# Optimization experiments

Hardware: AMD Instinct MI355X
Metric: run time of the kernel (lower is better)

## Reference

```python
import jax, jax.numpy as jnp
import numpy as np
import math

H = 512        # hidden_dim
DEPTH = 5
KS = 3         # kernel size
DELTA = 0.1
M = 104        # timestamp == seq_len
NC = 5
B = 512
BN_EPS = 1e-5


def setup_inputs() -> dict:
    key = jax.random.key(0)
    ks = jax.random.split(key, 16)
    inp = {}
    inp['x'] = jax.random.normal(ks[0], (B, 1, M), dtype=jnp.float32)
    # CausalCNN: depth conv layers (first is 1->H, rest H->H), each followed by BN
    inp['conv_w0'] = jax.random.normal(ks[1], (H, 1, KS), dtype=jnp.float32) * (1.0 / np.sqrt(KS))
    inp['conv_b0'] = jnp.zeros((H,), jnp.float32)
    inp['conv_w'] = jax.random.normal(ks[2], (DEPTH - 1, H, H, KS), dtype=jnp.float32) * (1.0 / np.sqrt(H * KS))
    inp['conv_b'] = jnp.zeros((DEPTH - 1, H), jnp.float32)
    inp['bn_gamma'] = jnp.ones((DEPTH, H), jnp.float32)
    inp['bn_beta'] = jnp.zeros((DEPTH, H), jnp.float32)
    # input_proj
    inp['proj_w'] = jax.random.normal(ks[3], (H, H), dtype=jnp.float32) * (1.0 / np.sqrt(H))
    inp['proj_b'] = jnp.zeros((H,), jnp.float32)
    # ZOH layers: A = -0.01*I + 0.001*randn, B = 0.01*randn [H,1], C = 0.01*randn [1,H]
    eye = jnp.eye(H, dtype=jnp.float32)
    inp['A_all'] = -0.01 * eye[None] + 0.001 * jax.random.normal(ks[4], (DEPTH, H, H), dtype=jnp.float32)
    inp['B_all'] = 0.01 * jax.random.normal(ks[5], (DEPTH, H, 1), dtype=jnp.float32)
    inp['C_all'] = 0.01 * jax.random.normal(ks[6], (DEPTH, 1, H), dtype=jnp.float32)
    # fc_temp: Linear(H,H) -> BN1d(H) -> GELU -> Dropout(eval) -> Linear(H,NC)
    inp['fc1_w'] = jax.random.normal(ks[7], (H, H), dtype=jnp.float32) * (1.0 / np.sqrt(H))
    inp['fc1_b'] = jnp.zeros((H,), jnp.float32)
    inp['fc_bn_gamma'] = jnp.ones((H,), jnp.float32)
    inp['fc_bn_beta'] = jnp.zeros((H,), jnp.float32)
    inp['fc2_w'] = jax.random.normal(ks[8], (NC, H), dtype=jnp.float32) * (1.0 / np.sqrt(H))
    inp['fc2_b'] = jnp.zeros((NC,), jnp.float32)
    return inp


def _causal_conv(x, w, b):
    # x: [B, Cin, T], w: [Cout, Cin, K] -> left-pad K-1 (equivalent to pad both + trim right)
    y = jax.lax.conv_general_dilated(x, w, window_strides=(1,), padding=[(KS - 1, 0)],
                                     dimension_numbers=('NCH', 'OIH', 'NCH'))
    return y + b[None, :, None]


def _bn_ct(x, g, b):
    # BatchNorm1d over [B, C, T], batch statistics (training-mode normalization)
    m = x.mean(axis=(0, 2), keepdims=True)
    v = x.var(axis=(0, 2), keepdims=True)
    return g[None, :, None] * (x - m) * jax.lax.rsqrt(v + BN_EPS) + b[None, :, None]


def _pos_encoding(T, d):
    pos = jnp.arange(T, dtype=jnp.float32)[:, None]
    div = jnp.exp(jnp.arange(0, d, 2, dtype=jnp.float32) * (-math.log(10000.0) / d))
    pe = jnp.zeros((T, d), jnp.float32)
    pe = pe.at[:, 0::2].set(jnp.sin(pos * div))
    pe = pe.at[:, 1::2].set(jnp.cos(pos * div))
    return pe


def _zoh_kbar(A, Bv, Cv):
    # A: [H,H], Bv: [H,1], Cv: [1,H] -> normalized K_bar [M]
    A_bar = jax.scipy.linalg.expm(DELTA * A)
    I = jnp.eye(H, dtype=A.dtype)
    A_inv = jnp.linalg.inv(A + 0.001 * I)
    B_bar = A_inv @ (A_bar - I) @ (DELTA * Bv)  # [H,1]
    # term_k = C @ A_bar^k @ B_bar; sequential vector recurrence replaces matrix powers
    def step(v, _):
        term = (Cv @ v)[0, 0]
        return A_bar @ v, term
    _, terms = jax.lax.scan(step, B_bar, None, length=M)  # [M]
    Kb = jnp.flip(terms, axis=0)
    return Kb / (jnp.linalg.norm(Kb) + 1e-6)


def reference(x, conv_w0, conv_b0, conv_w, conv_b, bn_gamma, bn_beta, proj_w, proj_b,
              A_all, B_all, C_all, fc1_w, fc1_b, fc_bn_gamma, fc_bn_beta, fc2_w, fc2_b):
    # CausalCNN
    h = jax.nn.relu(_bn_ct(_causal_conv(x, conv_w0, conv_b0), bn_gamma[0], bn_beta[0]))
    for i in range(DEPTH - 1):
        h = jax.nn.relu(_bn_ct(_causal_conv(h, conv_w[i], conv_b[i]), bn_gamma[i + 1], bn_beta[i + 1]))
    h = jnp.transpose(h, (0, 2, 1))  # [B, T, H]
    # positional encoding + input projection
    h = h + _pos_encoding(M, H)[None]
    h = jnp.einsum('bth,oh->bto', h, proj_w) + proj_b
    # stacked ZOH kernels: each layer multiplies x by its normalized K_bar along time
    Ks = jax.vmap(_zoh_kbar)(A_all, B_all, C_all)  # [DEPTH, M]
    h = h * jnp.prod(Ks, axis=0)[None, :, None]
    # mean pool over time, then fc_temp (BN with batch stats, dropout = identity/eval)
    h = h.mean(axis=1)  # [B, H]
    h = jnp.dot(h, fc1_w.T) + fc1_b
    m = h.mean(axis=0, keepdims=True)
    v = h.var(axis=0, keepdims=True)
    h = fc_bn_gamma * (h - m) * jax.lax.rsqrt(v + BN_EPS) + fc_bn_beta
    h = jax.nn.gelu(h, approximate=False)
    logits = jnp.dot(h, fc2_w.T) + fc2_b  # [B, NC]
    return logits
```

## Files before the change

kernel.cpp:

```cpp
#include <hip/hip_runtime.h>
#include <cstdio>
#include <cmath>
#include <cstdint>

constexpr int BM = 512 * 104;
constexpr float BN_EPS = 1e-5f;

constexpr size_t SZ_BF   = (size_t)BM * 512 * 2;
constexpr size_t SZ_MAT5 = (size_t)5 * 512 * 512 * 4;
constexpr size_t OFF_YB0 = 0;
constexpr size_t OFF_YB1 = OFF_YB0 + SZ_BF;
constexpr size_t OFF_WT2 = OFF_YB1 + SZ_BF;
constexpr size_t OFF_X   = OFF_WT2 + 6291456;
constexpr size_t OFF_T1  = OFF_X   + SZ_MAT5;
constexpr size_t OFF_T2  = OFF_T1  + SZ_MAT5;
constexpr size_t OFF_E   = OFF_T2  + SZ_MAT5;
constexpr size_t OFF_MW  = OFF_E   + SZ_MAT5;
constexpr size_t OFF_P2  = OFF_MW  + SZ_MAT5;
constexpr size_t OFF_P4  = OFF_P2  + SZ_MAT5;
constexpr size_t OFF_ROWT= OFF_P4  + SZ_MAT5;
constexpr size_t OFF_COLS= OFF_ROWT + 655360;
constexpr size_t OFF_COLS2=OFF_COLS + 655360;
constexpr size_t OFF_PIVI= OFF_COLS2 + 655360;
constexpr size_t OFF_PJT = OFF_PIVI + 81920;
constexpr size_t OFF_F1T = OFF_PJT + 1048576;
constexpr size_t OFF_G   = OFF_F1T + 1048576;
constexpr size_t OFF_POOL= OFF_G   + 1048576;
constexpr size_t OFF_Z   = OFF_POOL + 1048576;
constexpr size_t OFF_ST  = OFF_Z   + 1048576;
constexpr size_t OFF_U   = OFF_ST  + 49152;
constexpr size_t OFF_SV  = OFF_U   + 10240;
constexpr size_t OFF_V   = OFF_SV  + 10240;
constexpr size_t OFF_WV  = OFF_V   + 81920;
constexpr size_t OFF_S   = OFF_WV  + 133120;
constexpr size_t WS_NEED = OFF_S + 512;

__device__ __forceinline__ float bf2f(unsigned short u) {
    union { uint32_t i; float f; } x; x.i = (uint32_t)u << 16; return x.f;
}
__device__ __forceinline__ unsigned short f2bf(float f) {
    union { float f; uint32_t i; } x; x.f = f;
    uint32_t r = x.i + 0x7FFFu + ((x.i >> 16) & 1u);
    return (unsigned short)(r >> 16);
}

typedef __bf16 bf16x8 __attribute__((ext_vector_type(8)));
typedef float  f32x4  __attribute__((ext_vector_type(4)));

__device__ __forceinline__ void gld16(const void* g, void* l) {
    __builtin_amdgcn_global_load_lds((const __attribute__((address_space(1))) uint32_t*)g,
                                     (__attribute__((address_space(3))) uint32_t*)l, 16, 0, 0);
}

__device__ __forceinline__ uint32_t bnrelu_pk(uint32_t u, float sc0, float sc1, float sh0, float sh1) {
    union { uint32_t i; float f; } a, b;
    a.i = u << 16;
    b.i = u & 0xFFFF0000u;
    float x0 = fmaxf(fmaf(a.f, sc0, sh0), 0.0f);
    float x1 = fmaxf(fmaf(b.f, sc1, sh1), 0.0f);
    uint32_t r;
    asm volatile("v_cvt_pk_bf16_f32 %0, %1, %2" : "=v"(r) : "v"(x0), "v"(x1));
    return r;
}

__global__ void k_pre(const float* __restrict__ W, unsigned short* __restrict__ Wt2,
                      const float* __restrict__ Aall, float* __restrict__ X, float* __restrict__ MW,
                      float* __restrict__ COLSa, const float* __restrict__ Call, float* __restrict__ WV,
                      const float* __restrict__ pin0, float* __restrict__ pout0,
                      const float* __restrict__ pin1, float* __restrict__ pout1,
                      const float* __restrict__ xin, const float* __restrict__ w0,
                      const float* __restrict__ b0, unsigned short* __restrict__ y0,
                      double* __restrict__ s1g, double* __restrict__ s2g)
{
    __shared__ float tile[64 * 68];
    int bid = blockIdx.x;
    int tid = threadIdx.x;
    if (bid < 2048) {
        int co = bid & 511, l = bid >> 9;
        const float* src = W + (long)(l * 512 + co) * 512 * 3;
        unsigned short* dst = Wt2 + (long)l * 3 * 262144 + ((long)co << 9);
        int v = (co >> 1) & 3;
#pragma unroll
        for (int q = 0; q < 2; ++q) {
            int ci = tid * 2 + q;
            int chunk = (ci >> 3) & 3;
            int di = (ci & ~31) + (((chunk ^ v) & 3) << 3) + (ci & 7);
            float f0 = src[ci * 3 + 0], f1 = src[ci * 3 + 1], f2 = src[ci * 3 + 2];
            dst[di] = f2bf(f0);
            dst[262144 + di] = f2bf(f1);
            dst[524288 + di] = f2bf(f2);
        }
        return;
    }
    if (bid < 7168) {
        long i = (long)(bid - 2048) * 256 + tid;
        float a = Aall[i];
        X[i] = 0.1f * a;
        int z = (int)(i >> 18);
        int rc = (int)(i & 262143);
        int r = rc >> 9, c = rc & 511;
        float mw = a + ((r == c) ? 0.001f : 0.0f);
        MW[i] = mw;
        if (c < 64) COLSa[(long)z * 32768 + r * 64 + c] = mw;
        if (i < 2560) WV[(i >> 9) * 6656 + (i & 511)] = Call[i];
        return;
    }
    if (bid < 7296) {
        int id = bid - 7168;
        int bx = id & 7, by = (id >> 3) & 7, zi = id >> 6;
        const float* in = zi ? pin1 : pin0;
        float* outp = zi ? pout1 : pout0;
        for (int it = 0; it < 4; ++it) {
            int s = it * 256 + tid;
            int r = s >> 4, c4 = (s & 15) * 4;
            *(float4*)&tile[r * 68 + c4] = *(const float4*)&in[(long)(bx * 64 + r) * 512 + by * 64 + c4];
        }
        __syncthreads();
        for (int it = 0; it < 4; ++it) {
            int s = it * 256 + tid;
            int r = s >> 4, c4 = (s & 15) * 4;
            float4 v;
            v.x = tile[(c4 + 0) * 68 + r];
            v.y = tile[(c4 + 1) * 68 + r];
            v.z = tile[(c4 + 2) * 68 + r];
            v.w = tile[(c4 + 3) * 68 + r];
            *(float4*)&outp[(long)(by * 64 + r) * 512 + bx * 64 + c4] = v;
        }
        return;
    }
    {
        int id = bid - 7296;
        int b = id & 511;
        int c = (id >> 9) * 256 + tid;
        float w_0 = w0[c * 3 + 0], w_1 = w0[c * 3 + 1], w_2 = w0[c * 3 + 2], bb = b0[c];
        const float* xb = xin + b * 104;
        unsigned short* yb = y0 + (long)b * 104 * 512 + c;
        float xm2 = 0.0f, xm1 = 0.0f;
        float s1 = 0.0f, s2 = 0.0f;
        for (int t = 0; t < 104; ++t) {
            float x0 = xb[t];
            float v = w_0 * xm2 + w_1 * xm1 + w_2 * x0 + bb;
            yb[t * 512] = f2bf(v);
            s1 += v; s2 += v * v;
            xm2 = xm1; xm1 = x0;
        }
        atomicAdd(&s1g[c], (double)s1);
        atomicAdd(&s2g[c], (double)s2);
    }
}

__global__ __launch_bounds__(256) void k_mm(
    const float* __restrict__ A, long sA, int lda,
    const float* __restrict__ Bm, long sB, int ldb,
    float* __restrict__ C, long sC, int ldc,
    int K, int mode,
    const float* __restrict__ aux, long sAux,
    const float* __restrict__ aux2, float* __restrict__ Cp,
    double* __restrict__ st1, double* __restrict__ st2, int pc)
{
    __shared__ float sm[2 * 32 * 68];
    float* As = sm;
    float* Bs = sm + 32 * 68;
    int z = blockIdx.z;
    A  += (long)z * sA;
    Bm += (long)z * sB;
    C  += (long)z * sC;
    if (aux) aux += (long)z * sAux;
    int m0 = blockIdx.x * 64, n0 = blockIdx.y * 64;
    int tid = threadIdx.x;
    int tx = tid & 15, ty = tid >> 4;
    float acc[4][4] = {};
    for (int k0 = 0; k0 < K; k0 += 32) {
        __syncthreads();
#pragma unroll
        for (int it = 0; it < 2; ++it) {
            int s = it * 256 + tid;
            int mm = s >> 3, k4 = (s & 7) * 4;
            float4 v = *(const float4*)&A[(long)(m0 + mm) * lda + k0 + k4];
            As[(k4 + 0) * 68 + mm] = v.x;
            As[(k4 + 1) * 68 + mm] = v.y;
            As[(k4 + 2) * 68 + mm] = v.z;
            As[(k4 + 3) * 68 + mm] = v.w;
        }
#pragma unroll
        for (int it = 0; it < 2; ++it) {
            int s = it * 256 + tid;
            int kk = s >> 4, n4 = (s & 15) * 4;
            *(float4*)&Bs[kk * 68 + n4] = *(const float4*)&Bm[(long)(k0 + kk) * ldb + n0 + n4];
        }
        __syncthreads();
#pragma unroll 8
        for (int kk = 0; kk < 32; ++kk) {
            float4 a = *(const float4*)&As[kk * 68 + ty * 4];
            float4 b = *(const float4*)&Bs[kk * 68 + tx * 4];
            float av[4] = {a.x, a.y, a.z, a.w};
            float bv[4] = {b.x, b.y, b.z, b.w};
#pragma unroll
            for (int i = 0; i < 4; ++i)
#pragma unroll
                for (int j = 0; j < 4; ++j)
                    acc[i][j] = fmaf(av[i], bv[j], acc[i][j]);
        }
    }
    float sc2 = (mode == 5) ? aux2[0] : 0.0f;
    float cs1[4] = {0, 0, 0, 0}, cs2[4] = {0, 0, 0, 0};
#pragma unroll
    for (int i = 0; i < 4; ++i) {
        int row = m0 + ty * 4 + i;
        int col0 = n0 + tx * 4;
        long base = (long)row * ldc + col0;
        float v[4];
#pragma unroll
        for (int j = 0; j < 4; ++j) v[j] = acc[i][j];
        if (mode == 1) {
            for (int j = 0; j < 4; ++j) {
                int col = col0 + j;
                v[j] = v[j] + 2.0f * aux[(long)row * 512 + col] + ((row == col) ? 1.0f : 0.0f);
            }
        } else if (mode == 2) {
            for (int j = 0; j < 4; ++j)
                v[j] = v[j] + aux[(long)row * 512 + col0 + j];
        } else if (mode == 5) {
            for (int j = 0; j < 4; ++j) v[j] += aux[col0 + j] * sc2;
        } else if (mode == 7) {
            float pv[4];
            for (int j = 0; j < 4; ++j) {
                int col = col0 + j;
                pv[j] = ((row == col) ? 0.5f : 0.0f) + aux[(long)row * 512 + col] * (1.0f / 6.0f)
                        + v[j] * (1.0f / 24.0f);
            }
            *(float4*)&Cp[base] = make_float4(pv[0], pv[1], pv[2], pv[3]);
        } else if (mode == 8) {
            for (int j = 0; j < 4; ++j) {
                v[j] += aux[col0 + j];
                cs1[j] += v[j]; cs2[j] += v[j] * v[j];
            }
        }
        *(float4*)&C[base] = make_float4(v[0], v[1], v[2], v[3]);
    }
    if (mode == 8) {
        __syncthreads();
        float* s1s = sm;
        float* s2s = sm + 1024;
#pragma unroll
        for (int j = 0; j < 4; ++j) {
            s1s[ty * 64 + tx * 4 + j] = cs1[j];
            s2s[ty * 64 + tx * 4 + j] = cs2[j];
        }
        __syncthreads();
        if (tid < 64) {
            double a = 0.0, b = 0.0;
#pragma unroll
            for (int t = 0; t < 16; ++t) { a += s1s[t * 64 + tid]; b += s2s[t * 64 + tid]; }
            atomicAdd(&st1[n0 + tid], a);
            atomicAdd(&st2[n0 + tid], b);
        }
    }
}

__global__ __launch_bounds__(256) void k_elim3(
    const float* __restrict__ MWin, float* __restrict__ MWout,
    const float* __restrict__ PIVI, float* __restrict__ PIVN,
    const float* __restrict__ COLSc, float* __restrict__ COLSn, int pc, int pcn)
{
    __shared__ float As[64 * 68];
    __shared__ float Rs[64 * 68];
    __shared__ float fv[64];
    __shared__ int perm[64];
    __shared__ int arr[64];
    __shared__ int pividx;
    __shared__ float dv;
    int z = blockIdx.z;
    MWin += (long)z * 262144; MWout += (long)z * 262144;
    PIVI += z * 4096; COLSc += (long)z * 32768; COLSn += (long)z * 32768;
    int m0 = blockIdx.x * 64, n0 = blockIdx.y * 64;
    int tid = threadIdx.x;
    int tx = tid & 15, ty = tid >> 4;

    if (n0 == pc) {
        for (int it = 0; it < 16; ++it) {
            int idx = it * 256 + tid;
            int r = idx >> 6, c = idx & 63;
            Rs[r * 68 + c] = PIVI[r * 64 + c];
        }
        __syncthreads();
    } else {
        {
            int m = tid >> 2, kb = (tid & 3) * 16;
#pragma unroll
            for (int u = 0; u < 4; ++u) {
                float4 v = *(const float4*)&PIVI[m * 64 + kb + u * 4];
                As[(kb + u * 4 + 0) * 68 + m] = v.x;
                As[(kb + u * 4 + 1) * 68 + m] = v.y;
                As[(kb + u * 4 + 2) * 68 + m] = v.z;
                As[(kb + u * 4 + 3) * 68 + m] = v.w;
            }
            int kr = tid >> 2, cb = (tid & 3) * 16;
#pragma unroll
            for (int u = 0; u < 4; ++u)
                *(float4*)&Rs[kr * 68 + cb + u * 4] =
                    *(const float4*)&MWin[(long)(pc + kr) * 512 + n0 + cb + u * 4];
        }
        __syncthreads();
        float acc1[4][4] = {};
#pragma unroll 8
        for (int kk = 0; kk < 64; ++kk) {
            float4 a = *(const float4*)&As[kk * 68 + ty * 4];
            float4 b = *(const float4*)&Rs[kk * 68 + tx * 4];
            float av[4] = {a.x, a.y, a.z, a.w};
            float bv[4] = {b.x, b.y, b.z, b.w};
#pragma unroll
            for (int i = 0; i < 4; ++i)
#pragma unroll
                for (int j = 0; j < 4; ++j)
                    acc1[i][j] = fmaf(av[i], bv[j], acc1[i][j]);
        }
        __syncthreads();
#pragma unroll
        for (int i = 0; i < 4; ++i)
#pragma unroll
            for (int j = 0; j < 4; ++j)
                Rs[(ty * 4 + i) * 68 + tx * 4 + j] = acc1[i][j];
        __syncthreads();
    }

    if (m0 == pc) {
        for (int it = 0; it < 16; ++it) {
            int idx = it * 256 + tid;
            int r = idx >> 6, c = idx & 63;
            float v = Rs[r * 68 + c];
            MWout[(long)(pc + r) * 512 + n0 + c] = v;
            if (n0 == pcn) COLSn[(pc + r) * 64 + c] = v;
        }
        return;
    }
    {
        int m = tid >> 2, kb = (tid & 3) * 16;
#pragma unroll
        for (int u = 0; u < 4; ++u) {
            float4 v = *(const float4*)&COLSc[(m0 + m) * 64 + kb + u * 4];
            As[(kb + u * 4 + 0) * 68 + m] = v.x;
            As[(kb + u * 4 + 1) * 68 + m] = v.y;
            As[(kb + u * 4 + 2) * 68 + m] = v.z;
            As[(kb + u * 4 + 3) * 68 + m] = v.w;
        }
    }
    __syncthreads();
    float acc[4][4] = {};
#pragma unroll 8
    for (int kk = 0; kk < 64; ++kk) {
        float4 a = *(const float4*)&As[kk * 68 + ty * 4];
        float4 b = *(const float4*)&Rs[kk * 68 + tx * 4];
        float av[4] = {a.x, a.y, a.z, a.w};
        float bv[4] = {b.x, b.y, b.z, b.w};
#pragma unroll
        for (int i = 0; i < 4; ++i)
#pragma unroll
            for (int j = 0; j < 4; ++j)
                acc[i][j] = fmaf(av[i], bv[j], acc[i][j]);
    }
    bool inP = (n0 == pc);
    float vsav[4][4];
#pragma unroll
    for (int i = 0; i < 4; ++i) {
        int row = m0 + ty * 4 + i;
        int col0 = n0 + tx * 4;
        long base = (long)row * 512 + col0;
        float ov[4] = {0.f, 0.f, 0.f, 0.f};
        if (!inP) {
            float4 oldv = *(const float4*)&MWin[base];
            ov[0] = oldv.x; ov[1] = oldv.y; ov[2] = oldv.z; ov[3] = oldv.w;
        }
        float v[4];
#pragma unroll
        for (int j = 0; j < 4; ++j) { v[j] = ov[j] - acc[i][j]; vsav[i][j] = v[j]; }
        *(float4*)&MWout[base] = make_float4(v[0], v[1], v[2], v[3]);
        if (n0 == pcn)
            *(float4*)&COLSn[row * 64 + (col0 - pcn)] = make_float4(v[0], v[1], v[2], v[3]);
    }

    if (!(m0 == pcn && n0 == pcn)) return;
    __syncthreads();
    float* mat = As;
#pragma unroll
    for (int i = 0; i < 4; ++i)
#pragma unroll
        for (int j = 0; j < 4; ++j)
            mat[(ty * 4 + i) * 65 + tx * 4 + j] = vsav[i][j];
    __syncthreads();
    for (int j = 0; j < 64; ++j) {
        if (tid < 64) {
            float v = (tid >= j) ? fabsf(mat[tid * 65 + j]) : -1.0f;
            int idx = tid;
#pragma unroll
            for (int off = 32; off; off >>= 1) {
                float ov = __shfl_down(v, off);
                int oi = __shfl_down(idx, off);
                if (ov > v) { v = ov; idx = oi; }
            }
            if (tid == 0) pividx = idx;
        }
        __syncthreads();
        int r = pividx;
        if (tid < 64) {
            if (r != j) {
                float tj = mat[j * 65 + tid], tr = mat[r * 65 + tid];
                mat[j * 65 + tid] = tr; mat[r * 65 + tid] = tj;
            }
            if (tid == 0) perm[j] = r;
        }
        __syncthreads();
        if (tid < 64) {
            float piv = mat[j * 65 + j];
            float d = 1.0f / piv;
            fv[tid] = mat[tid * 65 + j];
            mat[j * 65 + tid] = (tid == j) ? d : mat[j * 65 + tid] * d;
            if (tid == 0) dv = d;
        }
        __syncthreads();
        {
            int i = tid & 63, c0 = (tid >> 6) * 16;
            if (i != j) {
                float f = fv[i];
                float dd = dv;
#pragma unroll
                for (int u = 0; u < 16; ++u) {
                    int c = c0 + u;
                    float val = mat[i * 65 + c] - f * mat[j * 65 + c];
                    if (c == j) val = -f * dd;
                    mat[i * 65 + c] = val;
                }
            }
        }
        __syncthreads();
    }
    if (tid == 0) {
        for (int c = 0; c < 64; ++c) arr[c] = c;
        for (int j = 63; j >= 0; --j) { int r = perm[j]; int t = arr[j]; arr[j] = arr[r]; arr[r] = t; }
    }
    __syncthreads();
    float* Pg = PIVN + z * 4096;
    for (int it = 0; it < 16; ++it) {
        int idx = it * 256 + tid;
        int r = idx >> 6, c = idx & 63;
        Pg[r * 64 + c] = mat[r * 65 + arr[c]];
    }
}

__global__ __launch_bounds__(256) void k_inv64(const float* __restrict__ MW, int pblk, float* __restrict__ PIVI)
{
    __shared__ float mat[64 * 65];
    __shared__ float fv[64];
    __shared__ int perm[64];
    __shared__ int arr[64];
    __shared__ int pividx;
    __shared__ float dv;
    int z = blockIdx.x;
    const float* Mg = MW + (long)z * 262144 + (long)pblk * 64 * 512 + pblk * 64;
    int tid = threadIdx.x;
    for (int it = 0; it < 16; ++it) {
        int idx = it * 256 + tid;
        int r = idx >> 6, c = idx & 63;
        mat[r * 65 + c] = Mg[r * 512 + c];
    }
    __syncthreads();
    for (int j = 0; j < 64; ++j) {
        if (tid < 64) {
            float v = (tid >= j) ? fabsf(mat[tid * 65 + j]) : -1.0f;
            int idx = tid;
#pragma unroll
            for (int off = 32; off; off >>= 1) {
                float ov = __shfl_down(v, off);
                int oi = __shfl_down(idx, off);
                if (ov > v) { v = ov; idx = oi; }
            }
            if (tid == 0) pividx = idx;
        }
        __syncthreads();
        int r = pividx;
        if (tid < 64) {
            if (r != j) {
                float tj = mat[j * 65 + tid], tr = mat[r * 65 + tid];
                mat[j * 65 + tid] = tr; mat[r * 65 + tid] = tj;
            }
            if (tid == 0) perm[j] = r;
        }
        __syncthreads();
        if (tid < 64) {
            float piv = mat[j * 65 + j];
            float d = 1.0f / piv;
            fv[tid] = mat[tid * 65 + j];
            mat[j * 65 + tid] = (tid == j) ? d : mat[j * 65 + tid] * d;
            if (tid == 0) dv = d;
        }
        __syncthreads();
        {
            int i = tid & 63, c0 = (tid >> 6) * 16;
            if (i != j) {
                float f = fv[i];
                float dd = dv;
#pragma unroll
                for (int u = 0; u < 16; ++u) {
                    int c = c0 + u;
                    float val = mat[i * 65 + c] - f * mat[j * 65 + c];
                    if (c == j) val = -f * dd;
                    mat[i * 65 + c] = val;
                }
            }
        }
        __syncthreads();
    }
    if (tid == 0) {
        for (int c = 0; c < 64; ++c) arr[c] = c;
        for (int j = 63; j >= 0; --j) { int r = perm[j]; int t = arr[j]; arr[j] = arr[r]; arr[r] = t; }
    }
    __syncthreads();
    float* Pg = PIVI + z * 4096;
    for (int it = 0; it < 16; ++it) {
        int idx = it * 256 + tid;
        int r = idx >> 6, c = idx & 63;
        Pg[r * 64 + c] = mat[r * 65 + arr[c]];
    }
}

__global__ void k_matvecA(const float* __restrict__ A, long sA,
                          const float* __restrict__ x, long sx,
                          float* __restrict__ y, long sy,
                          const float* __restrict__ sub, long ssub,
                          float alpha, float beta, int accum)
{
    int row = blockIdx.x, z = blockIdx.y, lane = threadIdx.x;
    A += (long)z * sA; x += (long)z * sx; y += (long)z * sy;
    if (sub) sub += (long)z * ssub;
    const float* ar = A + (long)row * 512;
    double acc = 0.0;
#pragma unroll
    for (int m = 0; m < 8; ++m) {
        int k = lane + m * 64;
        acc += (double)ar[k] * (double)x[k];
    }
    for (int off = 32; off; off >>= 1) acc += __shfl_down(acc, off);
    if (lane == 0) {
        float val = alpha * (float)acc + beta * x[row];
        if (sub) val = sub[row] - val;
        if (accum) y[row] += val; else y[row] = val;
    }
}

struct VWT { long a[8]; long x[8]; long y[8]; float al[8]; float be[8]; int ty[8]; };
__global__ void k_vw(const char* __restrict__ ws, VWT T)
{
    int g = blockIdx.x, z = blockIdx.y, t = blockIdx.z;
    int lane = threadIdx.x;
    const float* A = (const float*)(ws + T.a[t]) + (long)z * 262144;
    int ty = T.ty[t];
    long vs = ty ? 6656 : 4096;
    const float* x = (const float*)(ws + T.x[t]) + (long)z * vs;
    float* yv = (float*)(ws + T.y[t]) + (long)z * vs;
    if (ty == 0) {
        float xm[8];
#pragma unroll
        for (int m = 0; m < 8; ++m) xm[m] = x[lane + m * 64];
        float alpha = T.al[t], beta = T.be[t];
        for (int r0 = 0; r0 < 64; ++r0) {
            int row = g * 64 + r0;
            const float* ar = A + (long)row * 512;
            double acc = 0.0;
#pragma unroll
            for (int m = 0; m < 8; ++m) acc += (double)ar[lane + m * 64] * (double)xm[m];
            for (int off = 32; off; off >>= 1) acc += __shfl_down(acc, off);
            if (lane == 0) yv[row] = alpha * (float)acc + beta * x[row];
        }
    } else {
        __shared__ float xl[512];
#pragma unroll
        for (int m = 0; m < 8; ++m) xl[lane + m * 64] = x[lane + m * 64];
        __syncthreads();
        int c = g * 64 + lane;
        double acc = 0.0;
#pragma unroll 8
        for (int j = 0; j < 512; ++j) acc += (double)A[(long)j * 512 + c] * (double)xl[j];
        yv[c] = (float)acc;
    }
}

__global__ __launch_bounds__(256, 2) void k_convm(
    const unsigned short* __restrict__ act,
    const unsigned short* __restrict__ Wt2,
    const float* __restrict__ bias,
    const double* __restrict__ STin,
    const float* __restrict__ gam, const float* __restrict__ bet,
    unsigned short* __restrict__ yout,
    double* __restrict__ s1g, double* __restrict__ s2g,
    const float* __restrict__ WVt, const float* __restrict__ Vt, float* __restrict__ SVECt)
{
    __shared__ __align__(16) unsigned short As[130 * 32];
    __shared__ __align__(16) unsigned short Bs[3 * 256 * 32];
    __shared__ float SCs[512];
    __shared__ float SHs[512];
    __shared__ float invk[5];
    __shared__ float redk[2];
    int tid = threadIdx.x;
    if (blockIdx.x == 416) {
        if (blockIdx.y != 0 || WVt == nullptr) return;
        float* tl = (float*)As;
        for (int t = tid; t < 520; t += 256) {
            int z = t / 104, d = t - z * 104;
            int j = d >> 3, i = d & 7;
            const float* wp = WVt + z * 6656 + j * 512;
            const float* vp = Vt + z * 4096 + i * 512;
            float acc = 0.0f;
#pragma unroll 8
            for (int k = 0; k < 512; ++k) acc += wp[k] * vp[k];
            tl[t] = acc;
        }
        __syncthreads();
        int lane = tid & 63;
        for (int g = tid >> 6; g < 5; g += 4) {
            float a = tl[g * 104 + lane]; a = a * a;
            if (lane < 40) { float b = tl[g * 104 + 64 + lane]; a += b * b; }
#pragma unroll
            for (int off = 32; off; off >>= 1) a += __shfl_down(a, off);
            if (lane == 0) invk[g] = 1.0f / (sqrtf(a) + 1e-6f);
        }
        __syncthreads();
        float s = 0.0f;
        if (tid < 104) {
            s = 1.0f;
            for (int l = 0; l < 5; ++l) s *= tl[l * 104 + (103 - tid)] * invk[l];
            SVECt[tid] = s;
        }
        if (tid < 128) {
            float v = (tid < 104) ? s : 0.0f;
#pragma unroll
            for (int off = 32; off; off >>= 1) v += __shfl_down(v, off);
            if ((tid & 63) == 0) redk[tid >> 6] = v;
        }
        __syncthreads();
        if (tid == 0) SVECt[104] = (redk[0] + redk[1]) * (1.0f / 104.0f);
        return;
    }
    int m0 = blockIdx.x * 128, co0 = blockIdx.y * 256;
    int w = tid >> 6, lane = tid & 63;
    int wr = (w >> 1) * 64, wc = (w & 1) * 128;
    int fr = lane & 15, quad = lane >> 4;

    const double invN = 1.0 / (double)BM;
    for (int c = tid; c < 512; c += 256) {
        double mn = STin[c] * invN;
        double var = STin[512 + c] * invN - mn * mn;
        double rs = 1.0 / sqrt(var + (double)BN_EPS);
        double scd = (double)gam[c] * rs;
        SCs[c] = (float)scd;
        SHs[c] = (float)((double)bet[c] - mn * scd);
    }

    bool valid[4][3];
#pragma unroll
    for (int i = 0; i < 4; ++i) {
        int R = m0 + wr + i * 16 + fr;
        int t = R % 104;
#pragma unroll
        for (int tau = 0; tau < 3; ++tau) valid[i][tau] = (t + tau >= 2);
    }

    int aoff[4][3];
#pragma unroll
    for (int i = 0; i < 4; ++i)
#pragma unroll
        for (int tau = 0; tau < 3; ++tau) {
            int r = wr + i * 16 + fr + tau;
            aoff[i][tau] = r * 32 + (((quad ^ (r >> 1)) & 3) << 3);
        }
    int boff[8];
#pragma unroll
    for (int j = 0; j < 8; ++j) {
        int rb = wc + j * 16 + fr;
        boff[j] = rb * 32 + (((quad ^ (rb >> 1)) & 3) << 3);
    }

    int ka = (tid & 3) * 8;
    int g0 = m0 - 2 + (tid >> 2); if (g0 < 0) g0 = 0;
    int g1 = m0 + 62 + (tid >> 2);
    int g2 = m0 + 126 + (tid >> 2);
    const unsigned short* pa0 = act + (long)g0 * 512 + ka;
    const unsigned short* pa1 = act + (long)g1 * 512 + ka;
    const unsigned short* pa2 = act + (long)g2 * 512 + ka;
    int wbase = (tid >> 2) * 32 + ((((tid & 3) ^ (tid >> 3)) & 3) << 3);
    const unsigned short* pbB = Wt2 + ((long)(co0 + (tid >> 2)) << 9) + ka;

    f32x4 zero4 = {0.f, 0.f, 0.f, 0.f};
    f32x4 acc[4][8];
#pragma unroll
    for (int i = 0; i < 4; ++i)
#pragma unroll
        for (int j = 0; j < 8; ++j) acc[i][j] = zero4;
    bf16x8 zer = {0, 0, 0, 0, 0, 0, 0, 0};

#pragma unroll 1
    for (int s = 0; s < 16; ++s) {
        int ci0 = s * 32;
        __syncthreads();
        uint4 va0 = *(const uint4*)(pa0 + ci0);
        uint4 va1 = *(const uint4*)(pa1 + ci0);
        uint4 va2;
        if (tid < 8) va2 = *(const uint4*)(pa2 + ci0);
#pragma unroll
        for (int tau = 0; tau < 3; ++tau)
#pragma unroll
            for (int it = 0; it < 4; ++it)
                gld16(pbB + tau * 262144 + it * 32768 + ci0, &Bs[(tau * 4 + it) * 2048 + tid * 8]);
        int cb = ci0 + ka;
        float4 s0 = *(const float4*)&SCs[cb], s1v = *(const float4*)&SCs[cb + 4];
        float4 h0 = *(const float4*)&SHs[cb], h1v = *(const float4*)&SHs[cb + 4];
        {
            uint4 pk;
            pk.x = bnrelu_pk(va0.x, s0.x, s0.y, h0.x, h0.y);
            pk.y = bnrelu_pk(va0.y, s0.z, s0.w, h0.z, h0.w);
            pk.z = bnrelu_pk(va0.z, s1v.x, s1v.y, h1v.x, h1v.y);
            pk.w = bnrelu_pk(va0.w, s1v.z, s1v.w, h1v.z, h1v.w);
            *(uint4*)&As[wbase] = pk;
            pk.x = bnrelu_pk(va1.x, s0.x, s0.y, h0.x, h0.y);
            pk.y = bnrelu_pk(va1.y, s0.z, s0.w, h0.z, h0.w);
            pk.z = bnrelu_pk(va1.z, s1v.x, s1v.y, h1v.x, h1v.y);
            pk.w = bnrelu_pk(va1.w, s1v.z, s1v.w, h1v.z, h1v.w);
            *(uint4*)&As[wbase + 2048] = pk;
            if (tid < 8) {
                pk.x = bnrelu_pk(va2.x, s0.x, s0.y, h0.x, h0.y);
                pk.y = bnrelu_pk(va2.y, s0.z, s0.w, h0.z, h0.w);
                pk.z = bnrelu_pk(va2.z, s1v.x, s1v.y, h1v.x, h1v.y);
                pk.w = bnrelu_pk(va2.w, s1v.z, s1v.w, h1v.z, h1v.w);
                *(uint4*)&As[wbase + 4096] = pk;
            }
        }
        __syncthreads();
#pragma unroll
        for (int tau = 0; tau < 3; ++tau) {
            bf16x8 af[4];
#pragma unroll
            for (int i = 0; i < 4; ++i) {
                bf16x8 raw = *(const bf16x8*)&As[aoff[i][tau]];
                af[i] = valid[i][tau] ? raw : zer;
            }
            bf16x8 bfr[8];
#pragma unroll
            for (int j = 0; j < 8; ++j)
                bfr[j] = *(const bf16x8*)&Bs[tau * 8192 + boff[j]];
#pragma unroll
            for (int i = 0; i < 4; ++i)
#pragma unroll
                for (int j = 0; j < 8; ++j)
                    acc[i][j] = __builtin_amdgcn_mfma_f32_16x16x32_bf16(af[i], bfr[j], acc[i][j], 0, 0, 0);
        }
    }
    float bcol[8], s1[8], s2[8];
#pragma unroll
    for (int jt = 0; jt < 8; ++jt) {
        bcol[jt] = bias[co0 + wc + jt * 16 + fr];
        s1[jt] = 0.0f; s2[jt] = 0.0f;
    }
#pragma unroll
    for (int i = 0; i < 4; ++i) {
        int rbase = m0 + wr + i * 16 + quad * 4;
#pragma unroll
        for (int jt = 0; jt < 8; ++jt) {
            int col = co0 + wc + jt * 16 + fr;
#pragma unroll
            for (int r = 0; r < 4; ++r) {
                float v = acc[i][jt][r] + bcol[jt];
                yout[(long)(rbase + r) * 512 + col] = f2bf(v);
                s1[jt] += v; s2[jt] += v * v;
            }
        }
    }
#pragma unroll
    for (int jt = 0; jt < 8; ++jt) {
        s1[jt] += __shfl_xor(s1[jt], 16); s1[jt] += __shfl_xor(s1[jt], 32);
        s2[jt] += __shfl_xor(s2[jt], 16); s2[jt] += __shfl_xor(s2[jt], 32);
    }
    __syncthreads();
    float* st = (float*)As;
    if (lane < 16) {
#pragma unroll
        for (int jt = 0; jt < 8; ++jt) {
            st[w * 128 + jt * 16 + lane] = s1[jt];
            st[512 + w * 128 + jt * 16 + lane] = s2[jt];
        }
    }
    __syncthreads();
    {
        int half = tid >> 7, cl = tid & 127;
        float a = st[half * 128 + cl] + st[(half + 2) * 128 + cl];
        float b = st[512 + half * 128 + cl] + st[512 + (half + 2) * 128 + cl];
        atomicAdd(&s1g[co0 + tid], (double)a);
        atomicAdd(&s2g[co0 + tid], (double)b);
    }
}

__global__ void k_pool(const unsigned short* __restrict__ y4, const double* __restrict__ ST4,
                       const float* __restrict__ gam, const float* __restrict__ bet,
                       const float* __restrict__ svec, float* __restrict__ g)
{
    __shared__ float sl[104];
    int b = blockIdx.x;
    int c = blockIdx.y * 256 + threadIdx.x;
    if (threadIdx.x < 104) sl[threadIdx.x] = svec[threadIdx.x];
    __syncthreads();
    const double invN = 1.0 / (double)BM;
    double mn = ST4[c] * invN;
    double var = ST4[512 + c] * invN - mn * mn;
    double rs = 1.0 / sqrt(var + (double)BN_EPS);
    double scd = (double)gam[c] * rs;
    float sc = (float)scd, sh = (float)((double)bet[c] - mn * scd);
    int he = c & ~1;
    float div = expf((float)he * (-0.017988946039015984f));
    float acc = 0.0f;
    const unsigned short* yb = y4 + (long)b * 104 * 512 + c;
    for (int t = 0; t < 104; ++t) {
        float v = bf2f(yb[t * 512]);
        float hn = fmaxf(fmaf(v, sc, sh), 0.0f);
        float arg = (float)t * div;
        float pe = (c & 1) ? cosf(arg) : sinf(arg);
        acc += sl[t] * (hn + pe);
    }
    g[(long)b * 512 + c] = acc * (1.0f / 104.0f);
}

__global__ __launch_bounds__(256) void k_final(const float* __restrict__ zin, const double* __restrict__ st,
                                               const float* __restrict__ gam, const float* __restrict__ bet,
                                               const float* __restrict__ w2, const float* __restrict__ b2,
                                               float* __restrict__ outp)
{
    __shared__ float red[256];
    int b = blockIdx.x, tid = threadIdx.x;
    int oo[2] = { tid, tid + 256 };
    float gv[2];
#pragma unroll
    for (int q = 0; q < 2; ++q) {
        int o = oo[q];
        double m = st[o] * (1.0 / 512.0);
        double var = st[512 + o] * (1.0 / 512.0) - m * m;
        double rs = 1.0 / sqrt(var + (double)BN_EPS);
        float xn = (float)(((double)zin[(long)b * 512 + o] - m) * rs * (double)gam[o] + (double)bet[o]);
        gv[q] = 0.5f * xn * (1.0f + erff(xn * 0.70710678118654752f));
    }
    for (int n = 0; n < 5; ++n) {
        float p = gv[0] * w2[n * 512 + oo[0]] + gv[1] * w2[n * 512 + oo[1]];
        red[tid] = p;
        __syncthreads();
        for (int off = 128; off; off >>= 1) { if (tid < off) red[tid] += red[tid + off]; __syncthreads(); }
        if (tid == 0) outp[b * 5 + n] = red[0] + b2[n];
        __syncthreads();
    }
}

static void mm(hipStream_t s, int Mt, int Nt, int z,
               const float* A, long sA, int lda,
               const float* B, long sB, int ldb,
               float* C, long sC, int ldc,
               int K, int mode,
               const float* aux = nullptr, long sAux = 0, const float* aux2 = nullptr,
               float* Cp = nullptr, double* st1 = nullptr, double* st2 = nullptr, int pc = 0)
{
    dim3 g(Mt, Nt, z);
    k_mm<<<g, 256, 0, s>>>(A, sA, lda, B, sB, ldb, C, sC, ldc, K, mode, aux, sAux, aux2, Cp, st1, st2, pc);
}

extern "C" void kernel_launch(void* const* d_in, const int* in_sizes, int n_in,
                              void* d_out, int out_size, void* d_ws, size_t ws_size,
                              hipStream_t stream)
{
    (void)in_sizes; (void)n_in; (void)out_size;
    const float* x       = (const float*)d_in[0];
    const float* conv_w0 = (const float*)d_in[1];
    const float* conv_b0 = (const float*)d_in[2];
    const float* conv_w  = (const float*)d_in[3];
    const float* conv_b  = (const float*)d_in[4];
    const float* bn_g    = (const float*)d_in[5];
    const float* bn_b    = (const float*)d_in[6];
    const float* proj_w  = (const float*)d_in[7];
    const float* proj_b  = (const float*)d_in[8];
    const float* A_all   = (const float*)d_in[9];
    const float* B_all   = (const float*)d_in[10];
    const float* C_all   = (const float*)d_in[11];
    const float* fc1_w   = (const float*)d_in[12];
    const float* fc1_b   = (const float*)d_in[13];
    const float* fbn_g   = (const float*)d_in[14];
    const float* fbn_b   = (const float*)d_in[15];
    const float* fc2_w   = (const float*)d_in[16];
    const float* fc2_b   = (const float*)d_in[17];
    float* outp = (float*)d_out;
    char* ws = (char*)d_ws;
    if (ws_size < WS_NEED) { printf("ws too small: %zu < %zu\n", ws_size, WS_NEED); return; }

    unsigned short* YB0 = (unsigned short*)(ws + OFF_YB0);
    unsigned short* YB1 = (unsigned short*)(ws + OFF_YB1);
    unsigned short* WT2 = (unsigned short*)(ws + OFF_WT2);
    float* Xb   = (float*)(ws + OFF_X);
    float* T1   = (float*)(ws + OFF_T1);
    float* T2   = (float*)(ws + OFF_T2);
    float* Eb   = (float*)(ws + OFF_E);
    float* MW   = (float*)(ws + OFF_MW);
    float* P2   = (float*)(ws + OFF_P2);
    float* P4   = (float*)(ws + OFF_P4);
    float* COLS1= (float*)(ws + OFF_COLS);
    float* COLS2= (float*)(ws + OFF_COLS2);
    float* PIVA = (float*)(ws + OFF_PIVI);
    float* PIVB = (float*)(ws + OFF_ROWT);
    float* PJT  = (float*)(ws + OFF_PJT);
    float* F1T  = (float*)(ws + OFF_F1T);
    float* G    = (float*)(ws + OFF_G);
    float* POOL = (float*)(ws + OFF_POOL);
    float* Zb   = (float*)(ws + OFF_Z);
    double* ST  = (double*)(ws + OFF_ST);
    float* U    = (float*)(ws + OFF_U);
    float* SV   = (float*)(ws + OFF_SV);
    float* V    = (float*)(ws + OFF_V);
    float* WV   = (float*)(ws + OFF_WV);
    float* SVEC = (float*)(ws + OFF_S);

    const long SM = 262144;
    hipMemsetAsync(ws + OFF_ST, 0, 49152, stream);

    k_pre<<<8320, 256, 0, stream>>>(conv_w, WT2, A_all, Xb, MW, COLS1, C_all, WV,
                                    proj_w, PJT, fc1_w, F1T,
                                    x, conv_w0, conv_b0, YB0, ST, ST + 512);

    {
        float* MB[2]  = { MW, P2 };
        float* PB[2]  = { PIVA, PIVB };
        k_inv64<<<5, 256, 0, stream>>>(MW, 0, PB[0]);
        for (int p = 0; p < 8; ++p) {
            int pc = p * 64;
            float* Cc = (p & 1) ? COLS2 : COLS1;
            float* Cn = (p & 1) ? COLS1 : COLS2;
            k_elim3<<<dim3(8, 8, 5), 256, 0, stream>>>(MB[p & 1], MB[(p + 1) & 1],
                                                       PB[p & 1], PB[(p + 1) & 1],
                                                       Cc, Cn, pc, pc + 64);
        }
    }
    mm(stream, 8, 8, 5, Xb, SM, 512, Xb, SM, 512, T2, SM, 512, 512, 7, Xb, SM, nullptr, T1);
    mm(stream, 8, 8, 5, T2, SM, 512, T1, SM, 512, Eb, SM, 512, 512, 2, Xb, SM);
    mm(stream, 8, 8, 5, Eb, SM, 512, Eb, SM, 512, Xb, SM, 512, 512, 1, Eb, SM);
    mm(stream, 8, 8, 5, Xb, SM, 512, Xb, SM, 512, T1, SM, 512, 512, 0);
    mm(stream, 8, 8, 5, T1, SM, 512, T1, SM, 512, T2, SM, 512, 512, 0);
    mm(stream, 8, 8, 5, T2, SM, 512, T2, SM, 512, P2, SM, 512, 512, 0);
    mm(stream, 8, 8, 5, P2, SM, 512, P2, SM, 512, P4, SM, 512, 512, 0);
    k_matvecA<<<dim3(512, 5), 64, 0, stream>>>(Eb, SM, B_all, 512, U, 512, nullptr, 0, 0.1f, 0.0f, 0);
    k_matvecA<<<dim3(512, 5), 64, 0, stream>>>(MW, SM, U, 512, V, 4096, nullptr, 0, 1.0f, 0.0f, 0);
    k_matvecA<<<dim3(512, 5), 64, 0, stream>>>(A_all, SM, V, 4096, SV, 512, U, 512, 1.0f, 0.001f, 0);
    k_matvecA<<<dim3(512, 5), 64, 0, stream>>>(MW, SM, SV, 512, V, 4096, nullptr, 0, 1.0f, 0.0f, 1);
    auto Voff = [](int i) { return (long)(OFF_V + (size_t)i * 2048); };
    auto Woff = [](int j) { return (long)(OFF_WV + (size_t)j * 2048); };
    {
        VWT T = {};
        T.a[0] = OFF_E;  T.x[0] = Voff(0); T.y[0] = Voff(1); T.al[0] = 1; T.be[0] = 1; T.ty[0] = 0;
        T.a[1] = OFF_T2; T.x[1] = Woff(0); T.y[1] = Woff(1); T.ty[1] = 1;
        k_vw<<<dim3(8, 5, 2), 64, 0, stream>>>(ws, T);
    }
    {
        VWT T = {};
        T.a[0] = OFF_X;  T.x[0] = Voff(0); T.y[0] = Voff(2); T.al[0] = 1; T.ty[0] = 0;
        T.a[1] = OFF_X;  T.x[1] = Voff(1); T.y[1] = Voff(3); T.al[1] = 1; T.ty[1] = 0;
        T.a[2] = OFF_P2; T.x[2] = Woff(0); T.y[2] = Woff(2); T.ty[2] = 1;
        T.a[3] = OFF_P2; T.x[3] = Woff(1); T.y[3] = Woff(3); T.ty[3] = 1;
        k_vw<<<dim3(8, 5, 4), 64, 0, stream>>>(ws, T);
    }
    {
        VWT T = {};
        for (int i = 0; i < 4; ++i) {
            T.a[i] = OFF_T1; T.x[i] = Voff(i); T.y[i] = Voff(4 + i); T.al[i] = 1; T.ty[i] = 0;
            T.a[4 + i] = OFF_P4; T.x[4 + i] = Woff(i); T.y[4 + i] = Woff(4 + i); T.ty[4 + i] = 1;
        }
        k_vw<<<dim3(8, 5, 8), 64, 0, stream>>>(ws, T);
    }
    {
        VWT T = {};
        for (int i = 0; i < 4; ++i) {
            T.a[i] = OFF_P4; T.x[i] = Woff(4 + i); T.y[i] = Woff(8 + i); T.ty[i] = 1;
        }
        k_vw<<<dim3(8, 5, 4), 64, 0, stream>>>(ws, T);
    }
    {
        VWT T = {};
        T.a[0] = OFF_P4; T.x[0] = Woff(8); T.y[0] = Woff(12); T.ty[0] = 1;
        k_vw<<<dim3(8, 5, 1), 64, 0, stream>>>(ws, T);
    }

    for (int l = 1; l <= 4; ++l) {
        unsigned short* inb  = (l & 1) ? YB0 : YB1;
        unsigned short* outb = (l & 1) ? YB1 : YB0;
        dim3 grid(l == 1 ? 417 : 416, 2);
        k_convm<<<grid, 256, 0, stream>>>(inb, WT2 + (size_t)(l - 1) * 3 * 262144,
                                          conv_b + (l - 1) * 512,
                                          ST + (l - 1) * 1024, bn_g + (l - 1) * 512, bn_b + (l - 1) * 512,
                                          outb, ST + l * 1024, ST + l * 1024 + 512,
                                          (l == 1) ? WV : nullptr, V, SVEC);
    }
    k_pool<<<dim3(512, 2), 256, 0, stream>>>(YB0, ST + 4 * 1024, bn_g + 4 * 512, bn_b + 4 * 512, SVEC, G);

    mm(stream, 8, 8, 1, G, 0, 512, PJT, 0, 512, POOL, 0, 512, 512, 5, proj_b, 0, SVEC + 104);
    mm(stream, 8, 8, 1, POOL, 0, 512, F1T, 0, 512, Zb, 0, 512, 512, 8, fc1_b, 0, nullptr, nullptr,
       ST + 5 * 1024, ST + 5 * 1024 + 512);
    k_final<<<512, 256, 0, stream>>>(Zb, ST + 5 * 1024, fbn_g, fbn_b, fc2_w, fc2_b, outp);
}
```

Baseline: 1.737 ms.

## Software-pipeline conv GEMM K-loop with double-buffered LDS and per-tap phases

The causal-conv GEMM main loop now double-buffers the A tile and the B weight tile in LDS and splits each K step into three per-tap phases. The weight load for the next tap and the BN/ReLU packing of the next A slice overlap with the MFMAs of the current tap. Activation global loads are prefetched two steps ahead into alternating registers. s_setprio is raised around the MFMA bursts. LDS footprint shrinks, since the B buffer drops from three taps to two single-tap buffers, but there are more barriers per step and register pressure rises, which risks occupancy at launch bound 2.

```diff
diff --git a/kernel.cpp b/kernel.cpp
--- a/kernel.cpp
+++ b/kernel.cpp
@@ -594,8 +594,8 @@
     double* __restrict__ s1g, double* __restrict__ s2g,
     const float* __restrict__ WVt, const float* __restrict__ Vt, float* __restrict__ SVECt)
 {
-    __shared__ __align__(16) unsigned short As[130 * 32];
-    __shared__ __align__(16) unsigned short Bs[3 * 256 * 32];
+    __shared__ __align__(16) unsigned short BsD[2][256 * 32];
+    __shared__ __align__(16) unsigned short AsD[2][130 * 32];
     __shared__ float SCs[512];
     __shared__ float SHs[512];
     __shared__ float invk[5];
@@ -603,7 +603,7 @@
     int tid = threadIdx.x;
     if (blockIdx.x == 416) {
         if (blockIdx.y != 0 || WVt == nullptr) return;
-        float* tl = (float*)As;
+        float* tl = (float*)AsD;
         for (int t = tid; t < 520; t += 256) {
             int z = t / 104, d = t - z * 104;
             int j = d >> 3, i = d & 7;
@@ -697,62 +697,90 @@
         for (int j = 0; j < 8; ++j) acc[i][j] = zero4;
     bf16x8 zer = {0, 0, 0, 0, 0, 0, 0, 0};
 
+    uint4 vA0, vA1, vA2, vB0, vB1, vB2;
+
+#define LOADA(v0_, v1_, v2_, s_) { int ci0 = (s_) * 32;                        \
+        v0_ = *(const uint4*)(pa0 + ci0);                                      \
+        v1_ = *(const uint4*)(pa1 + ci0);                                      \
+        if (tid < 8) v2_ = *(const uint4*)(pa2 + ci0); }
+
+#define GLDB(tau_, s_, buf_) { int ci0 = (s_) * 32;                            \
+        _Pragma("unroll")                                                      \
+        for (int it = 0; it < 4; ++it)                                         \
+            gld16(pbB + (tau_) * 262144 + it * 32768 + ci0,                    \
+                  &BsD[buf_][it * 2048 + tid * 8]); }
+
+#define BNW(v0_, v1_, v2_, ab_, s_) { int cb = (s_) * 32 + ka;                 \
+        float4 s0 = *(const float4*)&SCs[cb], s1v = *(const float4*)&SCs[cb + 4]; \
+        float4 h0 = *(const float4*)&SHs[cb], h1v = *(const float4*)&SHs[cb + 4]; \
+        uint4 pk;                                                              \
+        pk.x = bnrelu_pk(v0_.x, s0.x, s0.y, h0.x, h0.y);                       \
+        pk.y = bnrelu_pk(v0_.y, s0.z, s0.w, h0.z, h0.w);                       \
+        pk.z = bnrelu_pk(v0_.z, s1v.x, s1v.y, h1v.x, h1v.y);                   \
+        pk.w = bnrelu_pk(v0_.w, s1v.z, s1v.w, h1v.z, h1v.w);                   \
+        *(uint4*)&AsD[ab_][wbase] = pk;                                        \
+        pk.x = bnrelu_pk(v1_.x, s0.x, s0.y, h0.x, h0.y);                       \
+        pk.y = bnrelu_pk(v1_.y, s0.z, s0.w, h0.z, h0.w);                       \
+        pk.z = bnrelu_pk(v1_.z, s1v.x, s1v.y, h1v.x, h1v.y);                   \
+        pk.w = bnrelu_pk(v1_.w, s1v.z, s1v.w, h1v.z, h1v.w);                   \
+        *(uint4*)&AsD[ab_][wbase + 2048] = pk;                                 \
+        if (tid < 8) {                                                         \
+            pk.x = bnrelu_pk(v2_.x, s0.x, s0.y, h0.x, h0.y);                   \
+            pk.y = bnrelu_pk(v2_.y, s0.z, s0.w, h0.z, h0.w);                   \
+            pk.z = bnrelu_pk(v2_.z, s1v.x, s1v.y, h1v.x, h1v.y);               \
+            pk.w = bnrelu_pk(v2_.w, s1v.z, s1v.w, h1v.z, h1v.w);               \
+            *(uint4*)&AsD[ab_][wbase + 4096] = pk; } }
+
+#define MFMA_PH(tau_, ab_, bbuf_) {                                            \
+        bf16x8 af[4];                                                          \
+        _Pragma("unroll")                                                      \
+        for (int i = 0; i < 4; ++i) {                                          \
+            bf16x8 raw = *(const bf16x8*)&AsD[ab_][aoff[i][tau_]];             \
+            af[i] = valid[i][tau_] ? raw : zer; }                              \
+        bf16x8 bfr[8];                                                         \
+        _Pragma("unroll")                                                      \
+        for (int j = 0; j < 8; ++j)                                            \
+            bfr[j] = *(const bf16x8*)&BsD[bbuf_][boff[j]];                     \
+        __builtin_amdgcn_s_setprio(1);                                         \
+        _Pragma("unroll")                                                      \
+        for (int i = 0; i < 4; ++i)                                            \
+            _Pragma("unroll")                                                  \
+            for (int j = 0; j < 8; ++j)                                        \
+                acc[i][j] = __builtin_amdgcn_mfma_f32_16x16x32_bf16(af[i], bfr[j], acc[i][j], 0, 0, 0); \
+        __builtin_amdgcn_s_setprio(0); }
+
+    LOADA(vA0, vA1, vA2, 0);
+    GLDB(0, 0, 0);
+    BNW(vA0, vA1, vA2, 0, 0);
+    LOADA(vB0, vB1, vB2, 1);
+    __syncthreads();
+
 #pragma unroll 1
     for (int s = 0; s < 16; ++s) {
-        int ci0 = s * 32;
-        __syncthreads();
-        uint4 va0 = *(const uint4*)(pa0 + ci0);
-        uint4 va1 = *(const uint4*)(pa1 + ci0);
-        uint4 va2;
-        if (tid < 8) va2 = *(const uint4*)(pa2 + ci0);
-#pragma unroll
-        for (int tau = 0; tau < 3; ++tau)
-#pragma unroll
-            for (int it = 0; it < 4; ++it)
-                gld16(pbB + tau * 262144 + it * 32768 + ci0, &Bs[(tau * 4 + it) * 2048 + tid * 8]);
-        int cb = ci0 + ka;
-        float4 s0 = *(const float4*)&SCs[cb], s1v = *(const float4*)&SCs[cb + 4];
-        float4 h0 = *(const float4*)&SHs[cb], h1v = *(const float4*)&SHs[cb + 4];
-        {
-            uint4 pk;
-            pk.x = bnrelu_pk(va0.x, s0.x, s0.y, h0.x, h0.y);
-            pk.y = bnrelu_pk(va0.y, s0.z, s0.w, h0.z, h0.w);
-            pk.z = bnrelu_pk(va0.z, s1v.x, s1v.y, h1v.x, h1v.y);
-            pk.w = bnrelu_pk(va0.w, s1v.z, s1v.w, h1v.z, h1v.w);
-            *(uint4*)&As[wbase] = pk;
-            pk.x = bnrelu_pk(va1.x, s0.x, s0.y, h0.x, h0.y);
-            pk.y = bnrelu_pk(va1.y, s0.z, s0.w, h0.z, h0.w);
-            pk.z = bnrelu_pk(va1.z, s1v.x, s1v.y, h1v.x, h1v.y);
-            pk.w = bnrelu_pk(va1.w, s1v.z, s1v.w, h1v.z, h1v.w);
-            *(uint4*)&As[wbase + 2048] = pk;
-            if (tid < 8) {
-                pk.x = bnrelu_pk(va2.x, s0.x, s0.y, h0.x, h0.y);
-                pk.y = bnrelu_pk(va2.y, s0.z, s0.w, h0.z, h0.w);
-                pk.z = bnrelu_pk(va2.z, s1v.x, s1v.y, h1v.x, h1v.y);
-                pk.w = bnrelu_pk(va2.w, s1v.z, s1v.w, h1v.z, h1v.w);
-                *(uint4*)&As[wbase + 4096] = pk;
-            }
-        }
-        __syncthreads();
-#pragma unroll
-        for (int tau = 0; tau < 3; ++tau) {
-            bf16x8 af[4];
-#pragma unroll
-            for (int i = 0; i < 4; ++i) {
-                bf16x8 raw = *(const bf16x8*)&As[aoff[i][tau]];
-                af[i] = valid[i][tau] ? raw : zer;
-            }
-            bf16x8 bfr[8];
-#pragma unroll
-            for (int j = 0; j < 8; ++j)
-                bfr[j] = *(const bf16x8*)&Bs[tau * 8192 + boff[j]];
-#pragma unroll
-            for (int i = 0; i < 4; ++i)
-#pragma unroll
-                for (int j = 0; j < 8; ++j)
-                    acc[i][j] = __builtin_amdgcn_mfma_f32_16x16x32_bf16(af[i], bfr[j], acc[i][j], 0, 0, 0);
-        }
-    }
+        int ab = s & 1;
+        GLDB(1, s, ab ^ 1);
+        MFMA_PH(0, ab, ab);
+        __syncthreads();
+        GLDB(2, s, ab);
+        if (s < 15) {
+            if (ab == 0) { BNW(vB0, vB1, vB2, 1, s + 1); }
+            else         { BNW(vA0, vA1, vA2, 0, s + 1); }
+        }
+        MFMA_PH(1, ab, ab ^ 1);
+        __syncthreads();
+        if (s < 15) GLDB(0, s + 1, ab ^ 1);
+        if (s < 14) {
+            if (ab == 0) { LOADA(vA0, vA1, vA2, s + 2); }
+            else         { LOADA(vB0, vB1, vB2, s + 2); }
+        }
+        MFMA_PH(2, ab, ab);
+        __syncthreads();
+    }
+#undef LOADA
+#undef GLDB
+#undef BNW
+#undef MFMA_PH
+
     float bcol[8], s1[8], s2[8];
 #pragma unroll
     for (int jt = 0; jt < 8; ++jt) {
@@ -779,7 +807,7 @@
         s2[jt] += __shfl_xor(s2[jt], 16); s2[jt] += __shfl_xor(s2[jt], 32);
     }
     __syncthreads();
-    float* st = (float*)As;
+    float* st = (float*)AsD;
     if (lane < 16) {
 #pragma unroll
         for (int jt = 0; jt < 8; ++jt) {
```

Result: slower. 1.772 ms (+2.0%).
